# Kernel optimization log

Hardware: AMD Instinct MI355X
Metric: run time of the kernel (lower is better)

Reference implementation:

```python
import jax, jax.numpy as jnp
import numpy as np

N_LR, N_HR = 25000, 100000
F_IN, F_W = 256, 512            # in_features, fnn_width
IN_MSG = F_W + 2 * F_IN         # 1024 (skip_connection=True)
LN_EPS = 1e-5


def _linear_init(key, out_f, in_f):
    # torch nn.Linear default: U(-1/sqrt(in_f), 1/sqrt(in_f)) for W and b
    kw, kb = jax.random.split(key)
    bound = 1.0 / np.sqrt(in_f)
    W = jax.random.uniform(kw, (out_f, in_f), jnp.float32, -bound, bound)
    b = jax.random.uniform(kb, (out_f,), jnp.float32, -bound, bound)
    return W, b


def setup_inputs() -> dict:
    key = jax.random.key(0)
    ks = jax.random.split(key, 12)
    v = jax.random.normal(ks[0], (N_LR, F_IN), jnp.float32)
    e_rel = jax.random.normal(ks[1], (N_HR, 1), jnp.float32)
    idx_hr_to_lr = jax.random.randint(ks[2], (N_HR,), 0, N_LR, jnp.int64)
    v_skip = jax.random.normal(ks[3], (N_HR, F_IN), jnp.float32)
    We, be = _linear_init(ks[4], F_W, 1)
    ln_g = jnp.ones((IN_MSG,), jnp.float32)
    ln_b = jnp.zeros((IN_MSG,), jnp.float32)
    W0, b0 = _linear_init(ks[5], F_W, IN_MSG)
    W1, b1 = _linear_init(ks[6], F_W, F_W)
    W2, b2 = _linear_init(ks[7], F_W, F_W)
    W3, b3 = _linear_init(ks[8], F_W, F_W)
    return dict(v=v, e_rel=e_rel, idx_hr_to_lr=idx_hr_to_lr, v_skip=v_skip,
                We=We, be=be, ln_g=ln_g, ln_b=ln_b,
                W0=W0, b0=b0, W1=W1, b1=b1, W2=W2, b2=b2, W3=W3, b3=b3)


def reference(v, e_rel, idx_hr_to_lr, v_skip, We, be, ln_g, ln_b,
              W0, b0, W1, b1, W2, b2, W3, b3):
    # edge encoder on negated relative positions: [N_hr, 1] -> [N_hr, F_W]
    e_enc = (-e_rel) @ We.T + be
    # gather low-res features + concat with skip features: [N_hr, IN_MSG]
    msg = jnp.concatenate([e_enc, v[idx_hr_to_lr], v_skip], axis=-1)
    # LayerNorm over last dim
    mu = jnp.mean(msg, axis=-1, keepdims=True)
    var = jnp.mean(jnp.square(msg - mu), axis=-1, keepdims=True)
    h = (msg - mu) * jax.lax.rsqrt(var + LN_EPS) * ln_g + ln_b
    # FNN: 4 linear+SELU layers (dropout=0)
    h = jax.nn.selu(h @ W0.T + b0)
    h = jax.nn.selu(h @ W1.T + b1)
    h = jax.nn.selu(h @ W2.T + b2)
    h = jax.nn.selu(h @ W3.T + b3)
    return h
```

## Files before the change

kernel.cpp:

```cpp
#include <hip/hip_runtime.h>

#define M_ROWS 100000
#define MPAD   100096
#define FW     512
#define INMSG  1024

typedef __attribute__((ext_vector_type(4))) float f32x4;
typedef __attribute__((ext_vector_type(8))) short bf16x8;

__device__ __forceinline__ unsigned short f2bf(float f) {
    unsigned u = __builtin_bit_cast(unsigned, f);
    u += 0x7fffu + ((u >> 16) & 1u);
    return (unsigned short)(u >> 16);
}

__device__ __forceinline__ float selu_f(float x) {
    const float scale = 1.0507009873554805f;
    const float alpha = 1.6732632423543772f;
    return scale * (x > 0.0f ? x : alpha * expm1f(x));
}

__global__ __launch_bounds__(256) void f32_to_bf16_k(
    const float* __restrict__ in, unsigned short* __restrict__ out, int n4)
{
    int i = blockIdx.x * 256 + threadIdx.x;
    if (i < n4) {
        f32x4 x = ((const f32x4*)in)[i];
        ushort4 o;
        o.x = f2bf(x[0]); o.y = f2bf(x[1]); o.z = f2bf(x[2]); o.w = f2bf(x[3]);
        ((ushort4*)out)[i] = o;
    }
}

__global__ __launch_bounds__(256) void build_msg_k(
    const float* __restrict__ v, const float* __restrict__ e_rel,
    const int* __restrict__ idx, const float* __restrict__ v_skip,
    const float* __restrict__ We, const float* __restrict__ be,
    const float* __restrict__ ln_g, const float* __restrict__ ln_b,
    unsigned short* __restrict__ msg)
{
    const int r = blockIdx.x;
    const int t = threadIdx.x;

    f32x4 val;
    if (t < 128) {
        float e = e_rel[r];
        f32x4 we = ((const f32x4*)We)[t];
        f32x4 bb = ((const f32x4*)be)[t];
        val = (-e) * we + bb;
    } else if (t < 192) {
        long vr = (long)idx[r] * 256;
        val = ((const f32x4*)(v + vr))[t - 128];
    } else {
        val = ((const f32x4*)(v_skip + (long)r * 256))[t - 192];
    }

    float s = val[0] + val[1] + val[2] + val[3];
    float q = val[0]*val[0] + val[1]*val[1] + val[2]*val[2] + val[3]*val[3];
    #pragma unroll
    for (int off = 32; off; off >>= 1) {
        s += __shfl_down(s, off, 64);
        q += __shfl_down(q, off, 64);
    }
    __shared__ float red[8];
    const int lane = t & 63, wv = t >> 6;
    if (lane == 0) { red[wv] = s; red[4 + wv] = q; }
    __syncthreads();
    float S  = red[0] + red[1] + red[2] + red[3];
    float Q  = red[4] + red[5] + red[6] + red[7];
    float mu = S * (1.0f / 1024.0f);
    float var = Q * (1.0f / 1024.0f) - mu * mu;
    float rs = rsqrtf(var + 1e-5f);

    f32x4 g = ((const f32x4*)ln_g)[t];
    f32x4 b = ((const f32x4*)ln_b)[t];
    ushort4 o;
    o.x = f2bf((val[0] - mu) * rs * g[0] + b[0]);
    o.y = f2bf((val[1] - mu) * rs * g[1] + b[1]);
    o.z = f2bf((val[2] - mu) * rs * g[2] + b[2]);
    o.w = f2bf((val[3] - mu) * rs * g[3] + b[3]);
    ((ushort4*)(msg + (long)r * INMSG))[t] = o;
}

template<int K, bool LAST>
__global__ __launch_bounds__(256) void gemm_selu_k(
    const unsigned short* __restrict__ A,
    const unsigned short* __restrict__ W,
    const float* __restrict__ bias,
    void* __restrict__ out, int M)
{
    __shared__ __align__(16) unsigned short ldsA[128][64];
    __shared__ __align__(16) unsigned short ldsB[128][64];

    const int tid  = threadIdx.x;
    const int lane = tid & 63;
    const int w    = tid >> 6;
    const int wr   = w >> 1, wc = w & 1;
    const long m0  = (long)blockIdx.x * 128;
    const int  n0  = blockIdx.y * 128;

    f32x4 acc[4][4] = {};

    const int lr = lane >> 3;
    const int lc = ((lane & 7) ^ lr) * 8;
    const int l15 = lane & 15;
    const int hi  = lane >> 4;
    const int l7  = lane & 7;

    for (int k0 = 0; k0 < K; k0 += 64) {
        #pragma unroll
        for (int i = 0; i < 4; ++i) {
            const int rowoff = i * 32 + w * 8;
            const unsigned short* ag = A + (m0 + rowoff + lr) * K + k0 + lc;
            __builtin_amdgcn_global_load_lds(
                (const __attribute__((address_space(1))) unsigned int*)ag,
                (__attribute__((address_space(3))) unsigned int*)&ldsA[rowoff][0],
                16, 0, 0);
            const unsigned short* bg = W + (long)(n0 + rowoff + lr) * K + k0 + lc;
            __builtin_amdgcn_global_load_lds(
                (const __attribute__((address_space(1))) unsigned int*)bg,
                (__attribute__((address_space(3))) unsigned int*)&ldsB[rowoff][0],
                16, 0, 0);
        }
        __syncthreads();

        #pragma unroll
        for (int kk = 0; kk < 2; ++kk) {
            bf16x8 af[4], bfr[4];
            #pragma unroll
            for (int mf = 0; mf < 4; ++mf) {
                const int g = (kk * 4 + hi) ^ l7;
                af[mf] = *(const bf16x8*)&ldsA[wr*64 + mf*16 + l15][g * 8];
            }
            #pragma unroll
            for (int nf = 0; nf < 4; ++nf) {
                const int g = (kk * 4 + hi) ^ l7;
                bfr[nf] = *(const bf16x8*)&ldsB[wc*64 + nf*16 + l15][g * 8];
            }
            #pragma unroll
            for (int mf = 0; mf < 4; ++mf)
                #pragma unroll
                for (int nf = 0; nf < 4; ++nf)
                    acc[mf][nf] = __builtin_amdgcn_mfma_f32_16x16x32_bf16(
                        af[mf], bfr[nf], acc[mf][nf], 0, 0, 0);
        }
        __syncthreads();
    }

    #pragma unroll
    for (int nf = 0; nf < 4; ++nf) {
        const int col = n0 + wc*64 + nf*16 + l15;
        const float bv = bias[col];
        #pragma unroll
        for (int mf = 0; mf < 4; ++mf) {
            const long row = m0 + wr*64 + mf*16 + hi * 4;
            #pragma unroll
            for (int i = 0; i < 4; ++i) {
                const long r = row + i;
                if (r < M) {
                    float x = acc[mf][nf][i] + bv;
                    float sv = selu_f(x);
                    if (LAST) ((float*)out)[r * FW + col] = sv;
                    else      ((unsigned short*)out)[r * FW + col] = f2bf(sv);
                }
            }
        }
    }
}

extern "C" void kernel_launch(void* const* d_in, const int* in_sizes, int n_in,
                              void* d_out, int out_size, void* d_ws, size_t ws_size,
                              hipStream_t stream) {
    const float* v      = (const float*)d_in[0];
    const float* e_rel  = (const float*)d_in[1];
    const int*   idx    = (const int*)d_in[2];
    const float* v_skip = (const float*)d_in[3];
    const float* We     = (const float*)d_in[4];
    const float* be     = (const float*)d_in[5];
    const float* ln_g   = (const float*)d_in[6];
    const float* ln_b   = (const float*)d_in[7];
    const float* W0 = (const float*)d_in[8];  const float* b0 = (const float*)d_in[9];
    const float* W1 = (const float*)d_in[10]; const float* b1 = (const float*)d_in[11];
    const float* W2 = (const float*)d_in[12]; const float* b2 = (const float*)d_in[13];
    const float* W3 = (const float*)d_in[14]; const float* b3 = (const float*)d_in[15];

    char* ws = (char*)d_ws;
    const size_t MSG_BYTES = (size_t)MPAD * INMSG * 2;
    const size_t H_BYTES   = (size_t)MPAD * FW * 2;
    unsigned short* msg = (unsigned short*)ws;
    unsigned short* W0b = (unsigned short*)(ws + MSG_BYTES);
    unsigned short* W1b = W0b + 1024 * 512;
    unsigned short* W2b = W1b + 512 * 512;
    unsigned short* W3b = W2b + 512 * 512;
    unsigned short* h0  = (unsigned short*)d_out;
    unsigned short* h1  = (unsigned short*)ws;
    unsigned short* h2  = (unsigned short*)(ws + H_BYTES);

    f32_to_bf16_k<<<dim3(512), 256, 0, stream>>>(W0, W0b, 1024 * 512 / 4);
    f32_to_bf16_k<<<dim3(256), 256, 0, stream>>>(W1, W1b, 512 * 512 / 4);
    f32_to_bf16_k<<<dim3(256), 256, 0, stream>>>(W2, W2b, 512 * 512 / 4);
    f32_to_bf16_k<<<dim3(256), 256, 0, stream>>>(W3, W3b, 512 * 512 / 4);

    build_msg_k<<<dim3(M_ROWS), 256, 0, stream>>>(v, e_rel, idx, v_skip,
                                                  We, be, ln_g, ln_b, msg);

    dim3 ggrid(MPAD / 128, FW / 128);
    gemm_selu_k<1024, false><<<ggrid, 256, 0, stream>>>(msg, W0b, b0, h0, M_ROWS);
    gemm_selu_k<512,  false><<<ggrid, 256, 0, stream>>>(h0,  W1b, b1, h1, M_ROWS);
    gemm_selu_k<512,  false><<<ggrid, 256, 0, stream>>>(h1,  W2b, b2, h2, M_ROWS);
    gemm_selu_k<512,  true ><<<ggrid, 256, 0, stream>>>(h2,  W3b, b3, d_out, M_ROWS);
}
```

Measured before the change: 1.212 ms.

## Double-buffer LDS tiles in GEMM and remap workgroups across XCDs

The GEMM now uses two LDS buffers, so the global-to-LDS load of the next K tile is issued while MFMAs run on the current one, with one barrier per iteration. The 2D grid becomes a 1D grid of 3128 workgroups. Each block index is remapped so consecutive tiles (four N tiles sharing an M row block) land on the same XCD, which should improve L2 reuse of A rows. This doubles LDS use per block, which may reduce occupancy. Correctness relies on the hardware ordering global_load_lds writes before the single barrier.

```diff
diff --git a/kernel.cpp b/kernel.cpp
--- a/kernel.cpp
+++ b/kernel.cpp
@@ -4,6 +4,10 @@
 #define MPAD   100096
 #define FW     512
 #define INMSG  1024
+#define NTILE  4
+#define MTILE  782
+#define NWG    3128
+#define CPX    391
 
 typedef __attribute__((ext_vector_type(4))) float f32x4;
 typedef __attribute__((ext_vector_type(8))) short bf16x8;
@@ -89,15 +93,18 @@
     const float* __restrict__ bias,
     void* __restrict__ out, int M)
 {
-    __shared__ __align__(16) unsigned short ldsA[128][64];
-    __shared__ __align__(16) unsigned short ldsB[128][64];
+    __shared__ __align__(16) unsigned short ldsA[2][128][64];
+    __shared__ __align__(16) unsigned short ldsB[2][128][64];
 
     const int tid  = threadIdx.x;
     const int lane = tid & 63;
     const int w    = tid >> 6;
     const int wr   = w >> 1, wc = w & 1;
-    const long m0  = (long)blockIdx.x * 128;
-    const int  n0  = blockIdx.y * 128;
+
+    const int b  = blockIdx.x;
+    const int l  = (b & 7) * CPX + (b >> 3);
+    const long m0 = (long)(l >> 2) * 128;
+    const int  n0 = (l & 3) * 128;
 
     f32x4 acc[4][4] = {};
 
@@ -107,36 +114,43 @@
     const int hi  = lane >> 4;
     const int l7  = lane & 7;
 
-    for (int k0 = 0; k0 < K; k0 += 64) {
+    const unsigned short* Abase = A + (m0 + w * 8 + lr) * K + lc;
+    const unsigned short* Bbase = W + (long)(n0 + w * 8 + lr) * K + lc;
+
+    auto stage = [&](int s, int t) {
+        const int k0 = t * 64;
         #pragma unroll
         for (int i = 0; i < 4; ++i) {
             const int rowoff = i * 32 + w * 8;
-            const unsigned short* ag = A + (m0 + rowoff + lr) * K + k0 + lc;
             __builtin_amdgcn_global_load_lds(
-                (const __attribute__((address_space(1))) unsigned int*)ag,
-                (__attribute__((address_space(3))) unsigned int*)&ldsA[rowoff][0],
+                (const __attribute__((address_space(1))) unsigned int*)(Abase + (long)i * 32 * K + k0),
+                (__attribute__((address_space(3))) unsigned int*)&ldsA[s][rowoff][0],
                 16, 0, 0);
-            const unsigned short* bg = W + (long)(n0 + rowoff + lr) * K + k0 + lc;
             __builtin_amdgcn_global_load_lds(
-                (const __attribute__((address_space(1))) unsigned int*)bg,
-                (__attribute__((address_space(3))) unsigned int*)&ldsB[rowoff][0],
+                (const __attribute__((address_space(1))) unsigned int*)(Bbase + (long)i * 32 * K + k0),
+                (__attribute__((address_space(3))) unsigned int*)&ldsB[s][rowoff][0],
                 16, 0, 0);
         }
-        __syncthreads();
+    };
+
+    constexpr int NT_K = K / 64;
+    stage(0, 0);
+    __syncthreads();
+
+    int cur = 0;
+    for (int t = 0; t < NT_K; ++t) {
+        if (t + 1 < NT_K) stage(cur ^ 1, t + 1);
 
         #pragma unroll
         for (int kk = 0; kk < 2; ++kk) {
             bf16x8 af[4], bfr[4];
-            #pragma unroll
-            for (int mf = 0; mf < 4; ++mf) {
-                const int g = (kk * 4 + hi) ^ l7;
-                af[mf] = *(const bf16x8*)&ldsA[wr*64 + mf*16 + l15][g * 8];
-            }
-            #pragma unroll
-            for (int nf = 0; nf < 4; ++nf) {
-                const int g = (kk * 4 + hi) ^ l7;
-                bfr[nf] = *(const bf16x8*)&ldsB[wc*64 + nf*16 + l15][g * 8];
-            }
+            const int g = (kk * 4 + hi) ^ l7;
+            #pragma unroll
+            for (int mf = 0; mf < 4; ++mf)
+                af[mf] = *(const bf16x8*)&ldsA[cur][wr*64 + mf*16 + l15][g * 8];
+            #pragma unroll
+            for (int nf = 0; nf < 4; ++nf)
+                bfr[nf] = *(const bf16x8*)&ldsB[cur][wc*64 + nf*16 + l15][g * 8];
             #pragma unroll
             for (int mf = 0; mf < 4; ++mf)
                 #pragma unroll
@@ -145,6 +159,7 @@
                         af[mf], bfr[nf], acc[mf][nf], 0, 0, 0);
         }
         __syncthreads();
+        cur ^= 1;
     }
 
     #pragma unroll
@@ -204,7 +219,7 @@
     build_msg_k<<<dim3(M_ROWS), 256, 0, stream>>>(v, e_rel, idx, v_skip,
                                                   We, be, ln_g, ln_b, msg);
 
-    dim3 ggrid(MPAD / 128, FW / 128);
+    dim3 ggrid(NWG);
     gemm_selu_k<1024, false><<<ggrid, 256, 0, stream>>>(msg, W0b, b0, h0, M_ROWS);
     gemm_selu_k<512,  false><<<ggrid, 256, 0, stream>>>(h0,  W1b, b1, h1, M_ROWS);
     gemm_selu_k<512,  false><<<ggrid, 256, 0, stream>>>(h1,  W2b, b2, h2, M_ROWS);
```

Measured after the change: 1.220 ms. About the same (+0.7%).
